# Kernel optimization log

Measured on AMD Instinct MI355X. Metric: run time of the kernel, lower is better.

Reference implementation:

```python
import jax, jax.numpy as jnp
import numpy as np

D = 256; HEADS = 8; HD = D // HEADS; LAYERS = 2
GS = 64; K = GS * GS; T = 4; P = 9; R = P // 2
B = 4; N = 511; H = 128; W = 128
SCALE = HD ** -0.5; SIGMA = 0.08


def _ln(x, g, b):
    m = jnp.mean(x, axis=-1, keepdims=True)
    v = jnp.var(x, axis=-1, keepdims=True)
    return (x - m) * jax.lax.rsqrt(v + 1e-5) * g + b


def _gelu(x):
    return jax.nn.gelu(x, approximate=False)  # torch nn.GELU default = exact erf


def _grid_xy():
    c = (jnp.arange(GS, dtype=jnp.float32) + 0.5) / GS
    gy, gx = jnp.meshgrid(c, c, indexing='ij')
    return jnp.stack([gx, gy], axis=-1).reshape(K, 2)  # (K,2)


def _patches(city, meas_xy):
    # city: (B,H,W), meas_xy: (B,N,2) -> (B,N,P,P)
    x = jnp.clip(jnp.round(meas_xy[..., 0] * (W - 1)).astype(jnp.int32), 0, W - 1)
    y = jnp.clip(jnp.round(meas_xy[..., 1] * (H - 1)).astype(jnp.int32), 0, H - 1)
    cp = jnp.pad(city, ((0, 0), (R, R), (R, R)))
    off = jnp.arange(P)  # = (-R..R) + R after padding
    yy = y[:, :, None, None] + off[None, None, :, None]
    xx = x[:, :, None, None] + off[None, None, None, :]
    bi = jnp.arange(B)[:, None, None, None]
    return cp[bi, yy, xx]


def _forward(meas_xy, meas_v, bs_xy, city, meas_W, meas_b, patch_W1, patch_b1,
             patch_W2, patch_b2, bs_W, bs_b, task_emb, taskp_W, taskp_b, grid_pos,
             lnq_g, lnq_b, lnkv_g, lnkv_b, qW, qb, kW, kb, vW, vb, oW, ob,
             dist_raw, dens_raw, lnf_g, lnf_b, f1W, f1b, f2W, f2b,
             tfp_W, tfp_b, head_W, head_b, task_id):
    # measurement tokens
    meas_in = jnp.concatenate([meas_xy, meas_v[..., None]], axis=-1)  # (B,N,3)
    meas_tok = meas_in @ meas_W + meas_b
    pf = _patches(city, meas_xy).reshape(B, N, P * P)
    pf = _gelu(pf @ patch_W1 + patch_b1) @ patch_W2 + patch_b2
    meas_tok = meas_tok + pf
    bs_tok = bs_xy @ bs_W + bs_b  # (B,1,D)
    src = jnp.concatenate([meas_tok, bs_tok], axis=1)          # (B,S,D)
    src_xy = jnp.concatenate([meas_xy, bs_xy], axis=1)         # (B,S,2)
    S = src.shape[1]

    gxy = _grid_xy()
    diff = gxy[None, :, None, :] - src_xy[:, None, :, :]       # (B,K,S,2)
    attn_bias = -jnp.sqrt(jnp.sum(diff * diff, axis=-1))       # (B,K,S)
    dm = gxy[None, :, None, :] - meas_xy[:, None, :, :]        # (B,K,N,2)
    density = jnp.mean(jnp.exp(-jnp.sum(dm * dm, axis=-1) / (2.0 * SIGMA * SIGMA)), axis=-1)  # (B,K)

    task_vec = (task_emb[task_id] @ taskp_W + taskp_b)[:, None, :]
    grid = grid_pos[None] + task_vec                           # (B,K,D)

    for i in range(LAYERS):
        q_in = _ln(grid, lnq_g[i], lnq_b[i])
        kv_in = _ln(src, lnkv_g[i], lnkv_b[i])
        q = (q_in @ qW[i] + qb[i]).reshape(B, K, HEADS, HD)
        k = (kv_in @ kW[i] + kb[i]).reshape(B, S, HEADS, HD)
        v = (kv_in @ vW[i] + vb[i]).reshape(B, S, HEADS, HD)
        scores = jnp.einsum('bkhd,bshd->bhks', q, k) * SCALE   # (B,H,K,S)
        scores = scores + jax.nn.softplus(dist_raw[i]) * attn_bias[:, None]
        gate = 1.0 + jnp.tanh(dens_raw[i]) * density[:, None, :, None]
        attn = jax.nn.softmax(scores * gate, axis=-1)
        out = jnp.einsum('bhks,bshd->bkhd', attn, v).reshape(B, K, D)
        grid = grid + out @ oW[i] + ob[i]
        hid = _ln(grid, lnf_g[i], lnf_b[i])
        grid = grid + _gelu(hid @ f1W[i] + f1b[i]) @ f2W[i] + f2b[i]

    tw = tfp_W[task_id]                                        # (B,D,D)
    tb = tfp_b[task_id]                                        # (B,D)
    tf = _gelu(jnp.einsum('bkd,bdh->bkh', grid, tw) + tb[:, None, :])
    logits = (tf @ head_W + head_b)[..., 0].reshape(B, GS, GS)
    return logits


def setup_inputs() -> dict:
    key = jax.random.key(0)
    ks = iter(jax.random.split(key, 48))
    def nrm(shape, s=0.02):
        return jax.random.normal(next(ks), shape, jnp.float32) * s
    inp = dict(
        meas_xy=jax.random.uniform(next(ks), (B, N, 2), jnp.float32),
        meas_v=jax.random.uniform(next(ks), (B, N), jnp.float32),
        bs_xy=jax.random.uniform(next(ks), (B, 1, 2), jnp.float32),
        city=jax.random.uniform(next(ks), (B, H, W), jnp.float32),
        meas_W=nrm((3, D)), meas_b=jnp.zeros(D),
        patch_W1=nrm((P * P, D)), patch_b1=jnp.zeros(D),
        patch_W2=nrm((D, D)), patch_b2=jnp.zeros(D),
        bs_W=nrm((2, D)), bs_b=jnp.zeros(D),
        task_emb=nrm((T, D), 1.0), taskp_W=nrm((D, D)), taskp_b=jnp.zeros(D),
        grid_pos=nrm((K, D)),
        lnq_g=jnp.ones((LAYERS, D)), lnq_b=jnp.zeros((LAYERS, D)),
        lnkv_g=jnp.ones((LAYERS, D)), lnkv_b=jnp.zeros((LAYERS, D)),
        qW=nrm((LAYERS, D, D)), qb=jnp.zeros((LAYERS, D)),
        kW=nrm((LAYERS, D, D)), kb=jnp.zeros((LAYERS, D)),
        vW=nrm((LAYERS, D, D)), vb=jnp.zeros((LAYERS, D)),
        oW=nrm((LAYERS, D, D)), ob=jnp.zeros((LAYERS, D)),
        dist_raw=nrm((LAYERS,), 0.5), dens_raw=nrm((LAYERS,), 0.5),
        lnf_g=jnp.ones((LAYERS, D)), lnf_b=jnp.zeros((LAYERS, D)),
        f1W=nrm((LAYERS, D, 2 * D)), f1b=jnp.zeros((LAYERS, 2 * D)),
        f2W=nrm((LAYERS, 2 * D, D)), f2b=jnp.zeros((LAYERS, D)),
        tfp_W=nrm((T, D, D)), tfp_b=jnp.zeros((T, D)),
        head_W=nrm((D, 1)), head_b=jnp.zeros(1),
        task_id=jax.random.randint(next(ks), (B,), 0, T),
    )
    return inp


def reference(meas_xy, meas_v, bs_xy, city, meas_W, meas_b, patch_W1, patch_b1,
              patch_W2, patch_b2, bs_W, bs_b, task_emb, taskp_W, taskp_b, grid_pos,
              lnq_g, lnq_b, lnkv_g, lnkv_b, qW, qb, kW, kb, vW, vb, oW, ob,
              dist_raw, dens_raw, lnf_g, lnf_b, f1W, f1b, f2W, f2b,
              tfp_W, tfp_b, head_W, head_b, task_id):
    return _forward(meas_xy, meas_v, bs_xy, city, meas_W, meas_b, patch_W1, patch_b1,
                    patch_W2, patch_b2, bs_W, bs_b, task_emb, taskp_W, taskp_b, grid_pos,
                    lnq_g, lnq_b, lnkv_g, lnkv_b, qW, qb, kW, kb, vW, vb, oW, ob,
                    dist_raw, dens_raw, lnf_g, lnf_b, f1W, f1b, f2W, f2b,
                    tfp_W, tfp_b, head_W, head_b, task_id)
```

## Files before the change

### kernel.cpp

```cpp
#include <hip/hip_runtime.h>
#include <hip/hip_fp16.h>
#include <math.h>

#define DD 256
#define NHEADS 8
#define HDIM 32
#define NLAYERS 2
#define GSZ 64
#define KGRID 4096
#define TTASK 4
#define BB 4
#define NMEAS 511
#define SSRC 512
#define HCITY 128
#define WCITY 128
#define ATT_SCALE 0.17677669529663687f
#define INV2S2 78.125f
#define LOG2E 1.4426950408889634f

typedef unsigned short u16;
typedef __attribute__((ext_vector_type(8))) short short8;
typedef __attribute__((ext_vector_type(4))) float f32x4;

__device__ __forceinline__ u16 f2bf(float f) {
    union { float f; unsigned int u; } x; x.f = f;
    return (u16)((x.u + 0x7fffu + ((x.u >> 16) & 1u)) >> 16);
}
__device__ __forceinline__ unsigned int cvtpk_bf16(float a, float b) {
    unsigned int r;
    asm("v_cvt_pk_bf16_f32 %0, %1, %2" : "=v"(r) : "v"(a), "v"(b));
    return r;
}
__device__ __forceinline__ float h2f(unsigned int u) {
    float r;
    asm("v_cvt_f32_f16 %0, %1" : "=v"(r) : "v"(u));
    return r;
}
__device__ __forceinline__ float gelu_f(float x) {
    return 0.5f * x * (1.0f + erff(x * 0.7071067811865476f));
}
__device__ __forceinline__ void gload16(const u16* g, u16* l) {
    __builtin_amdgcn_global_load_lds(
        (__attribute__((address_space(1))) void*)g,
        (__attribute__((address_space(3))) void*)l, 16, 0, 0);
}

__global__ void task_vec_kernel(const float* __restrict__ task_emb,
                                const float* __restrict__ tpW,
                                const float* __restrict__ tpb,
                                const int* __restrict__ task_id,
                                float* __restrict__ tv) {
    int b = blockIdx.x, t = threadIdx.x;
    int id = task_id[b];
    float a = tpb[t];
    for (int e = 0; e < DD; e++) a = fmaf(task_emb[id * DD + e], tpW[e * DD + t], a);
    tv[b * DD + t] = a;
}

__global__ void grid_init_kernel(const float* __restrict__ grid_pos,
                                 const float* __restrict__ tv,
                                 float* __restrict__ g) {
    int f = blockIdx.x * 256 + threadIdx.x;
    int b = f >> 18;
    float4 gp = ((const float4*)grid_pos)[f & 262143];
    float4 tvv = ((const float4*)tv)[b * 64 + (f & 63)];
    float4 o; o.x = gp.x + tvv.x; o.y = gp.y + tvv.y; o.z = gp.z + tvv.z; o.w = gp.w + tvv.w;
    ((float4*)g)[f] = o;
}

__global__ __launch_bounds__(256) void src_build_kernel(
    const float* __restrict__ meas_xy, const float* __restrict__ meas_v,
    const float* __restrict__ bs_xy, const float* __restrict__ city,
    const float* __restrict__ meas_W, const float* __restrict__ meas_b,
    const float* __restrict__ pW1, const float* __restrict__ pb1,
    const float* __restrict__ pW2, const float* __restrict__ pb2,
    const float* __restrict__ bs_W, const float* __restrict__ bs_b,
    float* __restrict__ src, float* __restrict__ src_xy) {
    __shared__ float sp[81];
    __shared__ float sh[DD];
    int b = blockIdx.x / SSRC, s = blockIdx.x % SSRC, t = threadIdx.x;
    if (s < NMEAS) {
        float mx = meas_xy[(b * NMEAS + s) * 2];
        float my = meas_xy[(b * NMEAS + s) * 2 + 1];
        float mv = meas_v[b * NMEAS + s];
        int cx = (int)rintf(mx * 127.0f); cx = min(max(cx, 0), 127);
        int cy = (int)rintf(my * 127.0f); cy = min(max(cy, 0), 127);
        if (t < 81) {
            int rr = cy + t / 9 - 4, cc = cx + t % 9 - 4;
            sp[t] = (rr >= 0 && rr < HCITY && cc >= 0 && cc < WCITY)
                        ? city[(b * HCITY + rr) * WCITY + cc] : 0.0f;
        }
        __syncthreads();
        float a1 = pb1[t];
        #pragma unroll 9
        for (int e = 0; e < 81; e++) a1 = fmaf(sp[e], pW1[e * DD + t], a1);
        sh[t] = gelu_f(a1);
        __syncthreads();
        float a2 = pb2[t];
        for (int e = 0; e < DD; e++) a2 = fmaf(sh[e], pW2[e * DD + t], a2);
        float mt = mx * meas_W[t] + my * meas_W[DD + t] + mv * meas_W[2 * DD + t] + meas_b[t];
        src[((size_t)(b * SSRC + s)) * DD + t] = mt + a2;
        if (t == 0) { src_xy[(b * SSRC + s) * 2] = mx; src_xy[(b * SSRC + s) * 2 + 1] = my; }
    } else {
        float bx = bs_xy[b * 2], by = bs_xy[b * 2 + 1];
        src[((size_t)(b * SSRC + s)) * DD + t] = bx * bs_W[t] + by * bs_W[DD + t] + bs_b[t];
        if (t == 0) { src_xy[(b * SSRC + s) * 2] = bx; src_xy[(b * SSRC + s) * 2 + 1] = by; }
    }
}

__global__ void density_kernel(const float* __restrict__ meas_xy, float* __restrict__ dens) {
    int w = threadIdx.x >> 6, lane = threadIdx.x & 63;
    int idx = blockIdx.x * 4 + w;
    int b = idx >> 12, k = idx & 4095;
    float gx = ((k & 63) + 0.5f) * (1.0f / 64.0f);
    float gy = ((k >> 6) + 0.5f) * (1.0f / 64.0f);
    float s = 0.0f;
    for (int n = lane; n < NMEAS; n += 64) {
        float2 xy = ((const float2*)meas_xy)[b * NMEAS + n];
        float dx = gx - xy.x, dy = gy - xy.y;
        s += __expf(-(dx * dx + dy * dy) * INV2S2);
    }
    #pragma unroll
    for (int o = 1; o < 64; o <<= 1) s += __shfl_xor(s, o, 64);
    if (lane == 0) dens[idx] = s * (1.0f / 511.0f);
}

__global__ void params_kernel(const float* __restrict__ dens,
                              const float* __restrict__ dist_raw,
                              const float* __restrict__ dens_raw,
                              const float* __restrict__ kb, const float* __restrict__ vb,
                              const float* __restrict__ hb,
                              float* __restrict__ gsc, float* __restrict__ gcc,
                              float* __restrict__ kvb, float* __restrict__ out) {
    int idx = blockIdx.x * 256 + threadIdx.x;
    int l = idx >> 14, i = idx & 16383;
    float gate = 1.0f + tanhf(dens_raw[l]) * dens[i];
    gsc[idx] = gate * ATT_SCALE * LOG2E;
    gcc[idx] = gate * log1pf(__expf(dist_raw[l])) * LOG2E;
    if (idx < 16384) out[idx] = hb[0];
    if (idx < 1024) {
        int ll = idx >> 9, c = idx & 511;
        kvb[idx] = (c < 256) ? kb[ll * 256 + c] : vb[ll * 256 + c - 256];
    }
}

__global__ __launch_bounds__(256) void dist_kernel(const float* __restrict__ sxy_g,
                                                   u16* __restrict__ dt) {
    __shared__ float2 sxy[SSRC];
    int bk = blockIdx.x;
    int b = bk >> 12, k = bk & 4095;
    int t = threadIdx.x;
    sxy[t]       = ((const float2*)sxy_g)[b * SSRC + t];
    sxy[t + 256] = ((const float2*)sxy_g)[b * SSRC + t + 256];
    __syncthreads();
    float gx = ((k & 63) + 0.5f) * (1.0f / 64.0f);
    float gy = ((k >> 6) + 0.5f) * (1.0f / 64.0f);
    float2 p0 = sxy[2 * t], p1 = sxy[2 * t + 1];
    float dx0 = gx - p0.x, dy0 = gy - p0.y;
    float dx1 = gx - p1.x, dy1 = gy - p1.y;
    float d0 = sqrtf(dx0 * dx0 + dy0 * dy0);
    float d1 = sqrtf(dx1 * dx1 + dy1 * dy1);
    __half h0 = __float2half(d0), h1 = __float2half(d1);
    unsigned int pk = (unsigned int)__half_as_ushort(h0) |
                      ((unsigned int)__half_as_ushort(h1) << 16);
    ((unsigned int*)dt)[(size_t)bk * 256 + t] = pk;
}

__global__ void ln_kernel(const float* __restrict__ X, const float* __restrict__ g,
                          const float* __restrict__ bvec, u16* __restrict__ Yb, int rows) {
    int w = threadIdx.x >> 6, lane = threadIdx.x & 63;
    int row = blockIdx.x * 4 + w;
    if (row >= rows) return;
    float4 x = ((const float4*)X)[(size_t)row * 64 + lane];
    float s = x.x + x.y + x.z + x.w;
    float q = x.x * x.x + x.y * x.y + x.z * x.z + x.w * x.w;
    #pragma unroll
    for (int o = 1; o < 64; o <<= 1) { s += __shfl_xor(s, o, 64); q += __shfl_xor(q, o, 64); }
    float m = s * (1.0f / 256.0f);
    float v = q * (1.0f / 256.0f) - m * m;
    float rs = rsqrtf(v + 1e-5f);
    float4 gg = ((const float4*)g)[lane], bb = ((const float4*)bvec)[lane];
    float4 y;
    y.x = (x.x - m) * rs * gg.x + bb.x;
    y.y = (x.y - m) * rs * gg.y + bb.y;
    y.z = (x.z - m) * rs * gg.z + bb.z;
    y.w = (x.w - m) * rs * gg.w + bb.w;
    uint2 o2;
    o2.x = cvtpk_bf16(y.x, y.y);
    o2.y = cvtpk_bf16(y.z, y.w);
    *(uint2*)&Yb[(size_t)row * 256 + lane * 4] = o2;
}

__global__ __launch_bounds__(256) void wconv_kernel(const float* __restrict__ W,
                                                    u16* __restrict__ Wt, int Kd, int Nd,
                                                    int ostride, int noff) {
    __shared__ float L[32][33];
    int z = blockIdx.z;
    size_t zin = (size_t)z * Kd * Nd;
    int n0 = blockIdx.x * 32, k0 = blockIdx.y * 32;
    int tx = threadIdx.x, ty = threadIdx.y;
    #pragma unroll
    for (int yy = 0; yy < 4; yy++)
        L[tx][ty + 8 * yy] = W[zin + (size_t)(k0 + ty + 8 * yy) * Nd + n0 + tx];
    __syncthreads();
    #pragma unroll
    for (int yy = 0; yy < 4; yy++)
        Wt[(size_t)z * ostride + (size_t)(noff + n0 + ty + 8 * yy) * Kd + k0 + tx] =
            f2bf(L[ty + 8 * yy][tx]);
}

__global__ __launch_bounds__(256) void vtrans_kernel(const u16* __restrict__ V,
                                                     u16* __restrict__ Vt,
                                                     int instride, int inoff) {
    __shared__ u16 L[32][33];
    int b = blockIdx.z;
    int n0 = blockIdx.x * 32, s0 = blockIdx.y * 32;
    int tx = threadIdx.x, ty = threadIdx.y;
    #pragma unroll
    for (int yy = 0; yy < 4; yy++)
        L[tx][ty + 8 * yy] = V[(size_t)(b * SSRC + s0 + ty + 8 * yy) * instride + inoff + n0 + tx];
    __syncthreads();
    #pragma unroll
    for (int yy = 0; yy < 4; yy++)
        Vt[(size_t)(b * DD + n0 + ty + 8 * yy) * SSRC + s0 + tx] = L[ty + 8 * yy][tx];
}

template <int ACT, int RES, int OBF, int OF32, int BATW, int RS, int HEAD, int KD>
__global__ __launch_bounds__(256) void gemm_glds(
    const u16* __restrict__ A, const u16* __restrict__ Wt,
    const float* __restrict__ bias, float* __restrict__ C, u16* __restrict__ Cb,
    int Nfull, const int* __restrict__ task_id, int wstride, int bstride,
    const float* __restrict__ rs, const float* __restrict__ hw) {
    __shared__ u16 sA[2][128][32];
    __shared__ u16 sB[2][128][32];
    int t = threadIdx.x;
    int w = t >> 6, lane = t & 63, lq = lane & 15, g = lane >> 4;
    int wr = w >> 1, wc = w & 1;
    int m0 = blockIdx.x * 128, n0 = blockIdx.y * 128;
    const u16* Wp = Wt;
    const float* bp = bias;
    if (BATW) {
        int id = task_id[m0 / KGRID];
        Wp += (size_t)id * wstride;
        bp += (size_t)id * bstride;
    }
    int srow = lane >> 2;
    int scol = (lane & 3) * 8;
    const u16* Ag0 = A  + (size_t)(m0 + w * 32 + srow) * KD + scol;
    const u16* Ag1 = Ag0 + (size_t)16 * KD;
    const u16* Bg0 = Wp + (size_t)(n0 + w * 32 + srow) * KD + scol;
    const u16* Bg1 = Bg0 + (size_t)16 * KD;

    f32x4 acc[4][4];
    #pragma unroll
    for (int fm = 0; fm < 4; fm++)
        #pragma unroll
        for (int fn = 0; fn < 4; fn++) acc[fm][fn] = {0.f, 0.f, 0.f, 0.f};

    const int NKS = KD / 32;
    gload16(Ag0, &sA[0][w * 32][0]);
    gload16(Ag1, &sA[0][w * 32 + 16][0]);
    gload16(Bg0, &sB[0][w * 32][0]);
    gload16(Bg1, &sB[0][w * 32 + 16][0]);
    __syncthreads();

    #pragma unroll
    for (int ks = 0; ks < NKS; ks++) {
        int cur = ks & 1;
        if (ks + 1 < NKS) {
            int ko = (ks + 1) * 32;
            gload16(Ag0 + ko, &sA[cur ^ 1][w * 32][0]);
            gload16(Ag1 + ko, &sA[cur ^ 1][w * 32 + 16][0]);
            gload16(Bg0 + ko, &sB[cur ^ 1][w * 32][0]);
            gload16(Bg1 + ko, &sB[cur ^ 1][w * 32 + 16][0]);
        }
        short8 af[4], bf[4];
        #pragma unroll
        for (int fm = 0; fm < 4; fm++)
            af[fm] = *(const short8*)&sA[cur][wr * 64 + fm * 16 + lq][g * 8];
        #pragma unroll
        for (int fn = 0; fn < 4; fn++)
            bf[fn] = *(const short8*)&sB[cur][wc * 64 + fn * 16 + lq][g * 8];
        #pragma unroll
        for (int fm = 0; fm < 4; fm++)
            #pragma unroll
            for (int fn = 0; fn < 4; fn++)
                acc[fm][fn] = __builtin_amdgcn_mfma_f32_16x16x32_bf16(af[fm], bf[fn], acc[fm][fn], 0, 0, 0);
        __syncthreads();
    }

    float hWv[4], bv[4];
    #pragma unroll
    for (int fn = 0; fn < 4; fn++) {
        int col = n0 + wc * 64 + fn * 16 + lq;
        bv[fn] = bp[col];
        if (HEAD) hWv[fn] = hw[col];
    }
    #pragma unroll
    for (int fm = 0; fm < 4; fm++) {
        int mbase = m0 + wr * 64 + fm * 16 + 4 * g;
        if (HEAD) {
            #pragma unroll
            for (int r = 0; r < 4; r++) {
                float part = 0.0f;
                #pragma unroll
                for (int fn = 0; fn < 4; fn++) {
                    float o = acc[fm][fn][r] + bv[fn];
                    if (ACT) o = gelu_f(o);
                    part = fmaf(o, hWv[fn], part);
                }
                part += __shfl_xor(part, 1, 64);
                part += __shfl_xor(part, 2, 64);
                part += __shfl_xor(part, 4, 64);
                part += __shfl_xor(part, 8, 64);
                if (lq == 0) atomicAdd(&C[mbase + r], part);
            }
        } else {
            #pragma unroll
            for (int fn = 0; fn < 4; fn++) {
                int col = n0 + wc * 64 + fn * 16 + lq;
                #pragma unroll
                for (int r = 0; r < 4; r++) {
                    float o = acc[fm][fn][r] + bv[fn];
                    if (RS) o *= rs[mbase + r];
                    if (ACT) o = gelu_f(o);
                    size_t off = (size_t)(mbase + r) * Nfull + col;
                    if (RES) o += C[off];
                    if (OF32) C[off] = o;
                    if (OBF) Cb[off] = f2bf(o);
                }
            }
        }
    }
}

#define DPAD 520
#define PSTR 40
__global__ __launch_bounds__(512) void attn_mfma_kernel(
    const u16* __restrict__ Qb, const u16* __restrict__ KVo, const u16* __restrict__ Vt,
    const u16* __restrict__ distT, const float* __restrict__ gccL,
    u16* __restrict__ O) {
    __shared__ u16 sD[32][DPAD];
    __shared__ u16 sP[16][16 * PSTR];
    int blk = blockIdx.x;
    int kt = blk & 127, b = blk >> 7;
    int t = threadIdx.x;
    {
        int r = t >> 4, cs = (t & 15) * 32;
        const u16* gp = distT + ((size_t)(b * KGRID) + kt * 32 + r) * SSRC + cs;
        uint4 d0 = *(const uint4*)gp;
        uint4 d1 = *(const uint4*)(gp + 8);
        uint4 d2 = *(const uint4*)(gp + 16);
        uint4 d3 = *(const uint4*)(gp + 24);
        *(uint4*)&sD[r][cs] = d0;
        *(uint4*)&sD[r][cs + 8] = d1;
        *(uint4*)&sD[r][cs + 16] = d2;
        *(uint4*)&sD[r][cs + 24] = d3;
    }
    __syncthreads();

    int w = t >> 6, lane = t & 63, lq = lane & 15, g = lane >> 4;
    int h = w;
    float gc[2];
    short8 qf[2];
    #pragma unroll
    for (int qc = 0; qc < 2; qc++) {
        int qrow = kt * 32 + qc * 16 + lq;
        gc[qc] = gccL[b * KGRID + qrow];
        qf[qc] = *(const short8*)(Qb + (size_t)(b * KGRID + qrow) * DD + h * HDIM + g * 8);
    }
    const u16* kbase = KVo + (size_t)(b * SSRC) * 512 + h * HDIM + g * 8;
    const u16* vbase = Vt + ((size_t)(b * NHEADS + h) * HDIM + lq) * SSRC + g * 8;

    f32x4 accA[2] = {{0.f, 0.f, 0.f, 0.f}, {0.f, 0.f, 0.f, 0.f}};
    f32x4 accB[2] = {{0.f, 0.f, 0.f, 0.f}, {0.f, 0.f, 0.f, 0.f}};
    f32x4 zero = {0.f, 0.f, 0.f, 0.f};
    float lsum[2] = {0.f, 0.f};

    for (int s0 = 0; s0 < SSRC; s0 += 32) {
        #pragma unroll
        for (int tl = 0; tl < 2; tl++) {
            int sb = s0 + tl * 16;
            short8 kf = *(const short8*)(kbase + (size_t)(sb + lq) * 512);
            #pragma unroll
            for (int qc = 0; qc < 2; qc++) {
                f32x4 c = __builtin_amdgcn_mfma_f32_16x16x32_bf16(kf, qf[qc], zero, 0, 0, 0);
                uint2 dh = *(const uint2*)&sD[qc * 16 + lq][sb + 4 * g];
                float p0 = exp2f(fmaf(-gc[qc], h2f(dh.x), c[0]));
                float p1 = exp2f(fmaf(-gc[qc], h2f(dh.x >> 16), c[1]));
                float p2 = exp2f(fmaf(-gc[qc], h2f(dh.y), c[2]));
                float p3 = exp2f(fmaf(-gc[qc], h2f(dh.y >> 16), c[3]));
                lsum[qc] += (p0 + p1) + (p2 + p3);
                int idx = lq * PSTR + tl * 16 + 4 * g;
                *(unsigned int*)&sP[w * 2 + qc][idx]     = cvtpk_bf16(p0, p1);
                *(unsigned int*)&sP[w * 2 + qc][idx + 2] = cvtpk_bf16(p2, p3);
            }
        }
        short8 v0 = *(const short8*)(vbase + s0);
        short8 v1 = *(const short8*)(vbase + 16 * SSRC + s0);
        #pragma unroll
        for (int qc = 0; qc < 2; qc++) {
            short8 pf = *(const short8*)&sP[w * 2 + qc][lq * PSTR + g * 8];
            accA[qc] = __builtin_amdgcn_mfma_f32_16x16x32_bf16(v0, pf, accA[qc], 0, 0, 0);
            accB[qc] = __builtin_amdgcn_mfma_f32_16x16x32_bf16(v1, pf, accB[qc], 0, 0, 0);
        }
    }

    #pragma unroll
    for (int qc = 0; qc < 2; qc++) {
        float ls = lsum[qc];
        ls += __shfl_xor(ls, 16, 64);
        ls += __shfl_xor(ls, 32, 64);
        float inv = 1.0f / ls;
        int qrow = kt * 32 + qc * 16 + lq;
        u16* op = O + (size_t)(b * KGRID + qrow) * DD + h * HDIM + 4 * g;
        uint2 o0, o1;
        o0.x = cvtpk_bf16(accA[qc][0] * inv, accA[qc][1] * inv);
        o0.y = cvtpk_bf16(accA[qc][2] * inv, accA[qc][3] * inv);
        o1.x = cvtpk_bf16(accB[qc][0] * inv, accB[qc][1] * inv);
        o1.y = cvtpk_bf16(accB[qc][2] * inv, accB[qc][3] * inv);
        *(uint2*)op = o0;
        *(uint2*)(op + 16) = o1;
    }
}

extern "C" void kernel_launch(void* const* d_in, const int* in_sizes, int n_in,
                              void* d_out, int out_size, void* d_ws, size_t ws_size,
                              hipStream_t stream) {
    const float* meas_xy = (const float*)d_in[0];
    const float* meas_v  = (const float*)d_in[1];
    const float* bs_xy   = (const float*)d_in[2];
    const float* city    = (const float*)d_in[3];
    const float* meas_W  = (const float*)d_in[4];
    const float* meas_b  = (const float*)d_in[5];
    const float* pW1     = (const float*)d_in[6];
    const float* pb1     = (const float*)d_in[7];
    const float* pW2     = (const float*)d_in[8];
    const float* pb2     = (const float*)d_in[9];
    const float* bs_W    = (const float*)d_in[10];
    const float* bs_b    = (const float*)d_in[11];
    const float* task_emb= (const float*)d_in[12];
    const float* taskp_W = (const float*)d_in[13];
    const float* taskp_b = (const float*)d_in[14];
    const float* grid_pos= (const float*)d_in[15];
    const float* lnq_g   = (const float*)d_in[16];
    const float* lnq_b   = (const float*)d_in[17];
    const float* lnkv_g  = (const float*)d_in[18];
    const float* lnkv_b  = (const float*)d_in[19];
    const float* qW      = (const float*)d_in[20];
    const float* qb      = (const float*)d_in[21];
    const float* kW      = (const float*)d_in[22];
    const float* kb      = (const float*)d_in[23];
    const float* vW      = (const float*)d_in[24];
    const float* vb      = (const float*)d_in[25];
    const float* oW      = (const float*)d_in[26];
    const float* ob      = (const float*)d_in[27];
    const float* dist_raw= (const float*)d_in[28];
    const float* dens_raw= (const float*)d_in[29];
    const float* lnf_g   = (const float*)d_in[30];
    const float* lnf_b   = (const float*)d_in[31];
    const float* f1W     = (const float*)d_in[32];
    const float* f1b     = (const float*)d_in[33];
    const float* f2W     = (const float*)d_in[34];
    const float* f2b     = (const float*)d_in[35];
    const float* tfp_W   = (const float*)d_in[36];
    const float* tfp_b   = (const float*)d_in[37];
    const float* head_W  = (const float*)d_in[38];
    const float* head_b  = (const float*)d_in[39];
    const int*   task_id = (const int*)d_in[40];

    float* ws = (float*)d_ws;
    float* src   = ws;
    float* gridb = src + 524288;
    float* distTf= gridb + 4194304;
    float* sxyb  = distTf + 4194304;
    float* densb = sxyb + 4096;
    float* tvec  = densb + 16384;
    float* gsc   = tvec + 1024;
    float* gcc   = gsc + 32768;
    float* kvb   = gcc + 32768;

    u16* distT = (u16*)distTf;

    u16* wtq  = (u16*)(kvb + 1024);
    u16* wto  = wtq  + 131072;
    u16* wkv  = wto  + 131072;
    u16* wtf1 = wkv  + 262144;
    u16* wtf2 = wtf1 + 262144;
    u16* wtt  = wtf2 + 262144;
    u16* kvbf = wtt  + 262144;
    u16* lnbf = kvbf + 524288;
    u16* qbf  = lnbf + 4194304;
    u16* kvo  = qbf  + 4194304;
    u16* vtbf = kvo  + 1048576;
    u16* obf  = vtbf + 524288;
    u16* fhbf = obf  + 4194304;

    const dim3 B32x8(32, 8);

    task_vec_kernel<<<BB, 256, 0, stream>>>(task_emb, taskp_W, taskp_b, task_id, tvec);
    grid_init_kernel<<<4096, 256, 0, stream>>>(grid_pos, tvec, gridb);
    src_build_kernel<<<BB * SSRC, 256, 0, stream>>>(meas_xy, meas_v, bs_xy, city,
                                                    meas_W, meas_b, pW1, pb1, pW2, pb2,
                                                    bs_W, bs_b, src, sxyb);
    density_kernel<<<4096, 256, 0, stream>>>(meas_xy, densb);
    params_kernel<<<128, 256, 0, stream>>>(densb, dist_raw, dens_raw, kb, vb, head_b,
                                           gsc, gcc, kvb, (float*)d_out);
    dist_kernel<<<BB * KGRID, 256, 0, stream>>>(sxyb, distT);

    wconv_kernel<<<dim3(8, 8, 2), B32x8, 0, stream>>>(qW, wtq, 256, 256, 65536, 0);
    wconv_kernel<<<dim3(8, 8, 2), B32x8, 0, stream>>>(kW, wkv, 256, 256, 131072, 0);
    wconv_kernel<<<dim3(8, 8, 2), B32x8, 0, stream>>>(vW, wkv, 256, 256, 131072, 256);
    wconv_kernel<<<dim3(8, 8, 2), B32x8, 0, stream>>>(oW, wto, 256, 256, 65536, 0);
    wconv_kernel<<<dim3(16, 8, 2), B32x8, 0, stream>>>(f1W, wtf1, 256, 512, 131072, 0);
    wconv_kernel<<<dim3(8, 16, 2), B32x8, 0, stream>>>(f2W, wtf2, 512, 256, 131072, 0);
    wconv_kernel<<<dim3(8, 8, 4), B32x8, 0, stream>>>(tfp_W, wtt, 256, 256, 65536, 0);

    for (int i = 0; i < NLAYERS; i++) {
        const int w16 = i * 65536, bso = i * DD;
        ln_kernel<<<512, 256, 0, stream>>>(src, lnkv_g + bso, lnkv_b + bso, kvbf, 2048);
        gemm_glds<0, 0, 1, 0, 0, 0, 0, 256><<<dim3(16, 4), 256, 0, stream>>>(
            kvbf, wkv + i * 131072, kvb + i * 512, nullptr, kvo, 512, nullptr, 0, 0, nullptr, nullptr);
        vtrans_kernel<<<dim3(8, 16, 4), B32x8, 0, stream>>>(kvo, vtbf, 512, 256);
        ln_kernel<<<4096, 256, 0, stream>>>(gridb, lnq_g + bso, lnq_b + bso, lnbf, 16384);
        gemm_glds<0, 0, 1, 0, 0, 1, 0, 256><<<dim3(128, 2), 256, 0, stream>>>(
            lnbf, wtq + w16, qb + bso, nullptr, qbf, 256, nullptr, 0, 0, gsc + i * 16384, nullptr);
        attn_mfma_kernel<<<BB * (KGRID / 32), 512, 0, stream>>>(
            qbf, kvo, vtbf, distT, gcc + i * 16384, obf);
        gemm_glds<0, 1, 0, 1, 0, 0, 0, 256><<<dim3(128, 2), 256, 0, stream>>>(
            obf, wto + w16, ob + bso, gridb, obf, 256, nullptr, 0, 0, nullptr, nullptr);
        ln_kernel<<<4096, 256, 0, stream>>>(gridb, lnf_g + bso, lnf_b + bso, lnbf, 16384);
        gemm_glds<1, 0, 1, 0, 0, 0, 0, 256><<<dim3(128, 4), 256, 0, stream>>>(
            lnbf, wtf1 + i * 131072, f1b + i * 512, nullptr, fhbf, 512, nullptr, 0, 0, nullptr, nullptr);
        gemm_glds<0, 1, 1, 1, 0, 0, 0, 512><<<dim3(128, 2), 256, 0, stream>>>(
            fhbf, wtf2 + i * 131072, f2b + bso, gridb, lnbf, 256, nullptr, 0, 0, nullptr, nullptr);
    }

    gemm_glds<1, 0, 0, 0, 1, 0, 1, 256><<<dim3(128, 2), 256, 0, stream>>>(
        lnbf, wtt, tfp_b, (float*)d_out, nullptr, 256, task_id, 65536, 256, nullptr, head_W);
}
```

Baseline: 478.9 us.

## Merge prep kernels and fuse KV/Q layernorm and projection launches

Folds the independent setup kernels (task vector, grid init, source build, density, distance table, params, seven weight conversions) into three multi-role kernels that dispatch by block index. Per layer, the KV and Q layernorms become one launch, and the KV and Q projection GEMMs become one launch sharing a common GEMM core. The aim is to cut kernel launch count and tail gaps so small independent jobs share one grid. The cost is larger grids with mixed block roles and some idle blocks in the combined GEMM grid.

Result: no change. 488.3 us (+2.0%).

```diff
diff --git a/kernel.cpp b/kernel.cpp
--- a/kernel.cpp
+++ b/kernel.cpp
@@ -45,40 +45,28 @@
         (__attribute__((address_space(3))) void*)l, 16, 0, 0);
 }
 
-__global__ void task_vec_kernel(const float* __restrict__ task_emb,
-                                const float* __restrict__ tpW,
-                                const float* __restrict__ tpb,
-                                const int* __restrict__ task_id,
-                                float* __restrict__ tv) {
-    int b = blockIdx.x, t = threadIdx.x;
-    int id = task_id[b];
-    float a = tpb[t];
-    for (int e = 0; e < DD; e++) a = fmaf(task_emb[id * DD + e], tpW[e * DD + t], a);
-    tv[b * DD + t] = a;
-}
-
-__global__ void grid_init_kernel(const float* __restrict__ grid_pos,
-                                 const float* __restrict__ tv,
-                                 float* __restrict__ g) {
-    int f = blockIdx.x * 256 + threadIdx.x;
-    int b = f >> 18;
-    float4 gp = ((const float4*)grid_pos)[f & 262143];
-    float4 tvv = ((const float4*)tv)[b * 64 + (f & 63)];
-    float4 o; o.x = gp.x + tvv.x; o.y = gp.y + tvv.y; o.z = gp.z + tvv.z; o.w = gp.w + tvv.w;
-    ((float4*)g)[f] = o;
-}
-
-__global__ __launch_bounds__(256) void src_build_kernel(
+__global__ __launch_bounds__(256) void prep1_kernel(
     const float* __restrict__ meas_xy, const float* __restrict__ meas_v,
     const float* __restrict__ bs_xy, const float* __restrict__ city,
     const float* __restrict__ meas_W, const float* __restrict__ meas_b,
     const float* __restrict__ pW1, const float* __restrict__ pb1,
     const float* __restrict__ pW2, const float* __restrict__ pb2,
     const float* __restrict__ bs_W, const float* __restrict__ bs_b,
-    float* __restrict__ src, float* __restrict__ src_xy) {
+    const float* __restrict__ task_emb, const float* __restrict__ tpW,
+    const float* __restrict__ tpb, const int* __restrict__ task_id,
+    float* __restrict__ src, float* __restrict__ src_xy, float* __restrict__ tv) {
     __shared__ float sp[81];
     __shared__ float sh[DD];
-    int b = blockIdx.x / SSRC, s = blockIdx.x % SSRC, t = threadIdx.x;
+    int blk = blockIdx.x, t = threadIdx.x;
+    if (blk >= BB * SSRC) {
+        int b = blk - BB * SSRC;
+        int id = task_id[b];
+        float a = tpb[t];
+        for (int e = 0; e < DD; e++) a = fmaf(task_emb[id * DD + e], tpW[e * DD + t], a);
+        tv[b * DD + t] = a;
+        return;
+    }
+    int b = blk / SSRC, s = blk % SSRC;
     if (s < NMEAS) {
         float mx = meas_xy[(b * NMEAS + s) * 2];
         float my = meas_xy[(b * NMEAS + s) * 2 + 1];
@@ -108,69 +96,122 @@
     }
 }
 
-__global__ void density_kernel(const float* __restrict__ meas_xy, float* __restrict__ dens) {
-    int w = threadIdx.x >> 6, lane = threadIdx.x & 63;
-    int idx = blockIdx.x * 4 + w;
-    int b = idx >> 12, k = idx & 4095;
-    float gx = ((k & 63) + 0.5f) * (1.0f / 64.0f);
-    float gy = ((k >> 6) + 0.5f) * (1.0f / 64.0f);
-    float s = 0.0f;
-    for (int n = lane; n < NMEAS; n += 64) {
-        float2 xy = ((const float2*)meas_xy)[b * NMEAS + n];
-        float dx = gx - xy.x, dy = gy - xy.y;
-        s += __expf(-(dx * dx + dy * dy) * INV2S2);
-    }
-    #pragma unroll
-    for (int o = 1; o < 64; o <<= 1) s += __shfl_xor(s, o, 64);
-    if (lane == 0) dens[idx] = s * (1.0f / 511.0f);
-}
-
-__global__ void params_kernel(const float* __restrict__ dens,
-                              const float* __restrict__ dist_raw,
-                              const float* __restrict__ dens_raw,
-                              const float* __restrict__ kb, const float* __restrict__ vb,
-                              const float* __restrict__ hb,
-                              float* __restrict__ gsc, float* __restrict__ gcc,
-                              float* __restrict__ kvb, float* __restrict__ out) {
-    int idx = blockIdx.x * 256 + threadIdx.x;
-    int l = idx >> 14, i = idx & 16383;
-    float gate = 1.0f + tanhf(dens_raw[l]) * dens[i];
-    gsc[idx] = gate * ATT_SCALE * LOG2E;
-    gcc[idx] = gate * log1pf(__expf(dist_raw[l])) * LOG2E;
-    if (idx < 16384) out[idx] = hb[0];
-    if (idx < 1024) {
-        int ll = idx >> 9, c = idx & 511;
-        kvb[idx] = (c < 256) ? kb[ll * 256 + c] : vb[ll * 256 + c - 256];
-    }
-}
-
-__global__ __launch_bounds__(256) void dist_kernel(const float* __restrict__ sxy_g,
-                                                   u16* __restrict__ dt) {
+__global__ __launch_bounds__(256) void prep2_kernel(
+    const float* __restrict__ grid_pos, const float* __restrict__ tv,
+    const float* __restrict__ meas_xy, const float* __restrict__ sxy_g,
+    float* __restrict__ g, float* __restrict__ dens, u16* __restrict__ dt) {
     __shared__ float2 sxy[SSRC];
-    int bk = blockIdx.x;
-    int b = bk >> 12, k = bk & 4095;
-    int t = threadIdx.x;
-    sxy[t]       = ((const float2*)sxy_g)[b * SSRC + t];
-    sxy[t + 256] = ((const float2*)sxy_g)[b * SSRC + t + 256];
+    int id = blockIdx.x, t = threadIdx.x;
+    if (id < 4096) {
+        int f = id * 256 + t;
+        int b = f >> 18;
+        float4 gp = ((const float4*)grid_pos)[f & 262143];
+        float4 tvv = ((const float4*)tv)[b * 64 + (f & 63)];
+        float4 o; o.x = gp.x + tvv.x; o.y = gp.y + tvv.y; o.z = gp.z + tvv.z; o.w = gp.w + tvv.w;
+        ((float4*)g)[f] = o;
+    } else if (id < 8192) {
+        int w = t >> 6, lane = t & 63;
+        int idx = (id - 4096) * 4 + w;
+        int b = idx >> 12, k = idx & 4095;
+        float gx = ((k & 63) + 0.5f) * (1.0f / 64.0f);
+        float gy = ((k >> 6) + 0.5f) * (1.0f / 64.0f);
+        float s = 0.0f;
+        for (int n = lane; n < NMEAS; n += 64) {
+            float2 xy = ((const float2*)meas_xy)[b * NMEAS + n];
+            float dx = gx - xy.x, dy = gy - xy.y;
+            s += __expf(-(dx * dx + dy * dy) * INV2S2);
+        }
+        #pragma unroll
+        for (int o = 1; o < 64; o <<= 1) s += __shfl_xor(s, o, 64);
+        if (lane == 0) dens[idx] = s * (1.0f / 511.0f);
+    } else {
+        int bk = id - 8192;
+        int b = bk >> 12, k = bk & 4095;
+        sxy[t]       = ((const float2*)sxy_g)[b * SSRC + t];
+        sxy[t + 256] = ((const float2*)sxy_g)[b * SSRC + t + 256];
+        __syncthreads();
+        float gx = ((k & 63) + 0.5f) * (1.0f / 64.0f);
+        float gy = ((k >> 6) + 0.5f) * (1.0f / 64.0f);
+        float2 p0 = sxy[2 * t], p1 = sxy[2 * t + 1];
+        float dx0 = gx - p0.x, dy0 = gy - p0.y;
+        float dx1 = gx - p1.x, dy1 = gy - p1.y;
+        float d0 = sqrtf(dx0 * dx0 + dy0 * dy0);
+        float d1 = sqrtf(dx1 * dx1 + dy1 * dy1);
+        __half h0 = __float2half(d0), h1 = __float2half(d1);
+        unsigned int pk = (unsigned int)__half_as_ushort(h0) |
+                          ((unsigned int)__half_as_ushort(h1) << 16);
+        ((unsigned int*)dt)[(size_t)bk * 256 + t] = pk;
+    }
+}
+
+__device__ __forceinline__ void wconv_body(const float* W, u16* Wt, int Kd, int Nd,
+                                           int ostride, int noff, int z, int n0, int k0,
+                                           int t, float* L) {
+    int tx = t & 31, ty = t >> 5;
+    size_t zin = (size_t)z * Kd * Nd;
+    #pragma unroll
+    for (int yy = 0; yy < 4; yy++)
+        L[tx * 33 + ty + 8 * yy] = W[zin + (size_t)(k0 + ty + 8 * yy) * Nd + n0 + tx];
     __syncthreads();
-    float gx = ((k & 63) + 0.5f) * (1.0f / 64.0f);
-    float gy = ((k >> 6) + 0.5f) * (1.0f / 64.0f);
-    float2 p0 = sxy[2 * t], p1 = sxy[2 * t + 1];
-    float dx0 = gx - p0.x, dy0 = gy - p0.y;
-    float dx1 = gx - p1.x, dy1 = gy - p1.y;
-    float d0 = sqrtf(dx0 * dx0 + dy0 * dy0);
-    float d1 = sqrtf(dx1 * dx1 + dy1 * dy1);
-    __half h0 = __float2half(d0), h1 = __float2half(d1);
-    unsigned int pk = (unsigned int)__half_as_ushort(h0) |
-                      ((unsigned int)__half_as_ushort(h1) << 16);
-    ((unsigned int*)dt)[(size_t)bk * 256 + t] = pk;
-}
-
-__global__ void ln_kernel(const float* __restrict__ X, const float* __restrict__ g,
-                          const float* __restrict__ bvec, u16* __restrict__ Yb, int rows) {
-    int w = threadIdx.x >> 6, lane = threadIdx.x & 63;
-    int row = blockIdx.x * 4 + w;
-    if (row >= rows) return;
+    #pragma unroll
+    for (int yy = 0; yy < 4; yy++)
+        Wt[(size_t)z * ostride + (size_t)(noff + n0 + ty + 8 * yy) * Kd + k0 + tx] =
+            f2bf(L[(ty + 8 * yy) * 33 + tx]);
+}
+
+__global__ __launch_bounds__(256) void prep3_kernel(
+    const float* __restrict__ qW, const float* __restrict__ kW,
+    const float* __restrict__ vW, const float* __restrict__ oW,
+    const float* __restrict__ f1W, const float* __restrict__ f2W,
+    const float* __restrict__ tfp_W,
+    u16* __restrict__ wtq, u16* __restrict__ wkv, u16* __restrict__ wto,
+    u16* __restrict__ wtf1, u16* __restrict__ wtf2, u16* __restrict__ wtt,
+    const float* __restrict__ dens, const float* __restrict__ dist_raw,
+    const float* __restrict__ dens_raw, const float* __restrict__ kb,
+    const float* __restrict__ vb, const float* __restrict__ hb,
+    float* __restrict__ gsc, float* __restrict__ gcc,
+    float* __restrict__ kvb, float* __restrict__ out) {
+    __shared__ float L[32 * 33];
+    int id = blockIdx.x, t = threadIdx.x;
+    if (id < 512) {
+        int seg = id >> 7, lid = id & 127;
+        int z = lid >> 6, rem = lid & 63;
+        int n0 = (rem & 7) * 32, k0 = (rem >> 3) * 32;
+        if (seg == 0)      wconv_body(qW, wtq, 256, 256, 65536, 0, z, n0, k0, t, L);
+        else if (seg == 1) wconv_body(kW, wkv, 256, 256, 131072, 0, z, n0, k0, t, L);
+        else if (seg == 2) wconv_body(vW, wkv, 256, 256, 131072, 256, z, n0, k0, t, L);
+        else               wconv_body(oW, wto, 256, 256, 65536, 0, z, n0, k0, t, L);
+    } else if (id < 768) {
+        int lid = id - 512;
+        int z = lid >> 7, rem = lid & 127;
+        int n0 = (rem & 15) * 32, k0 = (rem >> 4) * 32;
+        wconv_body(f1W, wtf1, 256, 512, 131072, 0, z, n0, k0, t, L);
+    } else if (id < 1024) {
+        int lid = id - 768;
+        int z = lid >> 7, rem = lid & 127;
+        int n0 = (rem & 7) * 32, k0 = (rem >> 3) * 32;
+        wconv_body(f2W, wtf2, 512, 256, 131072, 0, z, n0, k0, t, L);
+    } else if (id < 1280) {
+        int lid = id - 1024;
+        int z = lid >> 6, rem = lid & 63;
+        int n0 = (rem & 7) * 32, k0 = (rem >> 3) * 32;
+        wconv_body(tfp_W, wtt, 256, 256, 65536, 0, z, n0, k0, t, L);
+    } else {
+        int idx = (id - 1280) * 256 + t;
+        int l = idx >> 14, i = idx & 16383;
+        float gate = 1.0f + tanhf(dens_raw[l]) * dens[i];
+        gsc[idx] = gate * ATT_SCALE * LOG2E;
+        gcc[idx] = gate * log1pf(__expf(dist_raw[l])) * LOG2E;
+        if (idx < 16384) out[idx] = hb[0];
+        if (idx < 1024) {
+            int ll = idx >> 9, c = idx & 511;
+            kvb[idx] = (c < 256) ? kb[ll * 256 + c] : vb[ll * 256 + c - 256];
+        }
+    }
+}
+
+__device__ __forceinline__ void ln_body(const float* X, const float* g,
+                                        const float* bvec, u16* Yb, int row, int lane) {
     float4 x = ((const float4*)X)[(size_t)row * 64 + lane];
     float s = x.x + x.y + x.z + x.w;
     float q = x.x * x.x + x.y * x.y + x.z * x.z + x.w * x.w;
@@ -191,22 +232,21 @@
     *(uint2*)&Yb[(size_t)row * 256 + lane * 4] = o2;
 }
 
-__global__ __launch_bounds__(256) void wconv_kernel(const float* __restrict__ W,
-                                                    u16* __restrict__ Wt, int Kd, int Nd,
-                                                    int ostride, int noff) {
-    __shared__ float L[32][33];
-    int z = blockIdx.z;
-    size_t zin = (size_t)z * Kd * Nd;
-    int n0 = blockIdx.x * 32, k0 = blockIdx.y * 32;
-    int tx = threadIdx.x, ty = threadIdx.y;
-    #pragma unroll
-    for (int yy = 0; yy < 4; yy++)
-        L[tx][ty + 8 * yy] = W[zin + (size_t)(k0 + ty + 8 * yy) * Nd + n0 + tx];
-    __syncthreads();
-    #pragma unroll
-    for (int yy = 0; yy < 4; yy++)
-        Wt[(size_t)z * ostride + (size_t)(noff + n0 + ty + 8 * yy) * Kd + k0 + tx] =
-            f2bf(L[ty + 8 * yy][tx]);
+__global__ void ln_kernel(const float* __restrict__ X, const float* __restrict__ g,
+                          const float* __restrict__ bvec, u16* __restrict__ Yb, int rows) {
+    int w = threadIdx.x >> 6, lane = threadIdx.x & 63;
+    int row = blockIdx.x * 4 + w;
+    if (row < rows) ln_body(X, g, bvec, Yb, row, lane);
+}
+
+__global__ void ln2_kernel(const float* __restrict__ Xkv, const float* __restrict__ gkv,
+                           const float* __restrict__ bkv, u16* __restrict__ Ykv,
+                           const float* __restrict__ Xq, const float* __restrict__ gq,
+                           const float* __restrict__ bq, u16* __restrict__ Yq) {
+    int w = threadIdx.x >> 6, lane = threadIdx.x & 63;
+    int blk = blockIdx.x;
+    if (blk < 512) ln_body(Xkv, gkv, bkv, Ykv, blk * 4 + w, lane);
+    else           ln_body(Xq, gq, bq, Yq, (blk - 512) * 4 + w, lane);
 }
 
 __global__ __launch_bounds__(256) void vtrans_kernel(const u16* __restrict__ V,
@@ -225,25 +265,14 @@
         Vt[(size_t)(b * DD + n0 + ty + 8 * yy) * SSRC + s0 + tx] = L[ty + 8 * yy][tx];
 }
 
-template <int ACT, int RES, int OBF, int OF32, int BATW, int RS, int HEAD, int KD>
-__global__ __launch_bounds__(256) void gemm_glds(
-    const u16* __restrict__ A, const u16* __restrict__ Wt,
-    const float* __restrict__ bias, float* __restrict__ C, u16* __restrict__ Cb,
-    int Nfull, const int* __restrict__ task_id, int wstride, int bstride,
-    const float* __restrict__ rs, const float* __restrict__ hw) {
-    __shared__ u16 sA[2][128][32];
-    __shared__ u16 sB[2][128][32];
+template <int ACT, int RES, int OBF, int OF32, int RS, int HEAD, int KD>
+__device__ __forceinline__ void gemm_core(
+    const u16* A, const u16* Wp, const float* bp, float* C, u16* Cb,
+    int Nfull, int m0, int n0, const float* rs, const float* hw,
+    u16 (*sA)[128][32], u16 (*sB)[128][32]) {
     int t = threadIdx.x;
     int w = t >> 6, lane = t & 63, lq = lane & 15, g = lane >> 4;
     int wr = w >> 1, wc = w & 1;
-    int m0 = blockIdx.x * 128, n0 = blockIdx.y * 128;
-    const u16* Wp = Wt;
-    const float* bp = bias;
-    if (BATW) {
-        int id = task_id[m0 / KGRID];
-        Wp += (size_t)id * wstride;
-        bp += (size_t)id * bstride;
-    }
     int srow = lane >> 2;
     int scol = (lane & 3) * 8;
     const u16* Ag0 = A  + (size_t)(m0 + w * 32 + srow) * KD + scol;
@@ -331,6 +360,45 @@
                 }
             }
         }
+    }
+}
+
+template <int ACT, int RES, int OBF, int OF32, int BATW, int RS, int HEAD, int KD>
+__global__ __launch_bounds__(256) void gemm_glds(
+    const u16* __restrict__ A, const u16* __restrict__ Wt,
+    const float* __restrict__ bias, float* __restrict__ C, u16* __restrict__ Cb,
+    int Nfull, const int* __restrict__ task_id, int wstride, int bstride,
+    const float* __restrict__ rs, const float* __restrict__ hw) {
+    __shared__ u16 sA[2][128][32];
+    __shared__ u16 sB[2][128][32];
+    int m0 = blockIdx.x * 128, n0 = blockIdx.y * 128;
+    const u16* Wp = Wt;
+    const float* bp = bias;
+    if (BATW) {
+        int id = task_id[m0 / KGRID];
+        Wp += (size_t)id * wstride;
+        bp += (size_t)id * bstride;
+    }
+    gemm_core<ACT, RES, OBF, OF32, RS, HEAD, KD>(A, Wp, bp, C, Cb, Nfull, m0, n0, rs, hw, sA, sB);
+}
+
+__global__ __launch_bounds__(256) void gemm_kvq_kernel(
+    const u16* __restrict__ kvbf, const u16* __restrict__ wkv,
+    const float* __restrict__ kvb, u16* __restrict__ kvo,
+    const u16* __restrict__ lnbf, const u16* __restrict__ wtq,
+    const float* __restrict__ qb, u16* __restrict__ qbf,
+    const float* __restrict__ gsc) {
+    __shared__ u16 sA[2][128][32];
+    __shared__ u16 sB[2][128][32];
+    if (blockIdx.y == 2) {
+        if (blockIdx.x >= 64) return;
+        int m0 = (blockIdx.x & 15) * 128, n0 = (blockIdx.x >> 4) * 128;
+        gemm_core<0, 0, 1, 0, 0, 0, 256>(kvbf, wkv, kvb, nullptr, kvo, 512, m0, n0,
+                                         nullptr, nullptr, sA, sB);
+    } else {
+        int m0 = blockIdx.x * 128, n0 = blockIdx.y * 128;
+        gemm_core<0, 0, 1, 0, 1, 0, 256>(lnbf, wtq, qb, nullptr, qbf, 256, m0, n0,
+                                         gsc, nullptr, sA, sB);
     }
 }
 
@@ -496,35 +564,23 @@
     u16* obf  = vtbf + 524288;
     u16* fhbf = obf  + 4194304;
 
-    const dim3 B32x8(32, 8);
-
-    task_vec_kernel<<<BB, 256, 0, stream>>>(task_emb, taskp_W, taskp_b, task_id, tvec);
-    grid_init_kernel<<<4096, 256, 0, stream>>>(grid_pos, tvec, gridb);
-    src_build_kernel<<<BB * SSRC, 256, 0, stream>>>(meas_xy, meas_v, bs_xy, city,
-                                                    meas_W, meas_b, pW1, pb1, pW2, pb2,
-                                                    bs_W, bs_b, src, sxyb);
-    density_kernel<<<4096, 256, 0, stream>>>(meas_xy, densb);
-    params_kernel<<<128, 256, 0, stream>>>(densb, dist_raw, dens_raw, kb, vb, head_b,
-                                           gsc, gcc, kvb, (float*)d_out);
-    dist_kernel<<<BB * KGRID, 256, 0, stream>>>(sxyb, distT);
-
-    wconv_kernel<<<dim3(8, 8, 2), B32x8, 0, stream>>>(qW, wtq, 256, 256, 65536, 0);
-    wconv_kernel<<<dim3(8, 8, 2), B32x8, 0, stream>>>(kW, wkv, 256, 256, 131072, 0);
-    wconv_kernel<<<dim3(8, 8, 2), B32x8, 0, stream>>>(vW, wkv, 256, 256, 131072, 256);
-    wconv_kernel<<<dim3(8, 8, 2), B32x8, 0, stream>>>(oW, wto, 256, 256, 65536, 0);
-    wconv_kernel<<<dim3(16, 8, 2), B32x8, 0, stream>>>(f1W, wtf1, 256, 512, 131072, 0);
-    wconv_kernel<<<dim3(8, 16, 2), B32x8, 0, stream>>>(f2W, wtf2, 512, 256, 131072, 0);
-    wconv_kernel<<<dim3(8, 8, 4), B32x8, 0, stream>>>(tfp_W, wtt, 256, 256, 65536, 0);
+    prep1_kernel<<<BB * SSRC + BB, 256, 0, stream>>>(
+        meas_xy, meas_v, bs_xy, city, meas_W, meas_b, pW1, pb1, pW2, pb2,
+        bs_W, bs_b, task_emb, taskp_W, taskp_b, task_id, src, sxyb, tvec);
+    prep2_kernel<<<24576, 256, 0, stream>>>(grid_pos, tvec, meas_xy, sxyb,
+                                            gridb, densb, distT);
+    prep3_kernel<<<1408, 256, 0, stream>>>(
+        qW, kW, vW, oW, f1W, f2W, tfp_W, wtq, wkv, wto, wtf1, wtf2, wtt,
+        densb, dist_raw, dens_raw, kb, vb, head_b, gsc, gcc, kvb, (float*)d_out);
 
     for (int i = 0; i < NLAYERS; i++) {
         const int w16 = i * 65536, bso = i * DD;
-        ln_kernel<<<512, 256, 0, stream>>>(src, lnkv_g + bso, lnkv_b + bso, kvbf, 2048);
-        gemm_glds<0, 0, 1, 0, 0, 0, 0, 256><<<dim3(16, 4), 256, 0, stream>>>(
-            kvbf, wkv + i * 131072, kvb + i * 512, nullptr, kvo, 512, nullptr, 0, 0, nullptr, nullptr);
-        vtrans_kernel<<<dim3(8, 16, 4), B32x8, 0, stream>>>(kvo, vtbf, 512, 256);
-        ln_kernel<<<4096, 256, 0, stream>>>(gridb, lnq_g + bso, lnq_b + bso, lnbf, 16384);
-        gemm_glds<0, 0, 1, 0, 0, 1, 0, 256><<<dim3(128, 2), 256, 0, stream>>>(
-            lnbf, wtq + w16, qb + bso, nullptr, qbf, 256, nullptr, 0, 0, gsc + i * 16384, nullptr);
+        ln2_kernel<<<4608, 256, 0, stream>>>(src, lnkv_g + bso, lnkv_b + bso, kvbf,
+                                             gridb, lnq_g + bso, lnq_b + bso, lnbf);
+        gemm_kvq_kernel<<<dim3(128, 3), 256, 0, stream>>>(
+            kvbf, wkv + i * 131072, kvb + i * 512, kvo,
+            lnbf, wtq + w16, qb + bso, qbf, gsc + i * 16384);
+        vtrans_kernel<<<dim3(8, 16, 4), dim3(32, 8), 0, stream>>>(kvo, vtbf, 512, 256);
         attn_mfma_kernel<<<BB * (KGRID / 32), 512, 0, stream>>>(
             qbf, kvo, vtbf, distT, gcc + i * 16384, obf);
         gemm_glds<0, 1, 0, 1, 0, 0, 0, 256><<<dim3(128, 2), 256, 0, stream>>>(
```
